# Kernel optimization log

Measured on AMD Instinct MI355X. Metric: run time of the kernel, lower is better.

Reference implementation:

```python
import jax, jax.numpy as jnp
import numpy as np

D_MODEL = 1024
N_HEADS = 16
HEAD_DIM = D_MODEL // N_HEADS


def setup_inputs() -> dict:
    key = jax.random.key(0)
    k0, k1, k2, k3, k4, k5 = jax.random.split(key, 6)
    s = 1.0 / np.sqrt(D_MODEL)
    return {
        "q": jax.random.normal(k0, (2, 2048, D_MODEL), dtype=jnp.float32),
        "Wq": jax.random.normal(k1, (D_MODEL, D_MODEL), dtype=jnp.float32) * s,
        "Wk": jax.random.normal(k2, (D_MODEL, D_MODEL), dtype=jnp.float32) * s,
        "Wv": jax.random.normal(k3, (D_MODEL, D_MODEL), dtype=jnp.float32) * s,
        "Wo": jax.random.normal(k4, (D_MODEL, D_MODEL), dtype=jnp.float32) * s,
        "bo": jax.random.normal(k5, (D_MODEL,), dtype=jnp.float32) * 0.01,
    }


def _split_heads(x):
    b, s, _ = x.shape
    return x.reshape(b, s, N_HEADS, HEAD_DIM).transpose(0, 2, 1, 3)  # [b,h,s,d]


def reference(q, Wq, Wk, Wv, Wo, bo):
    # self-attention: k = v = q
    qh = _split_heads(q @ Wq)  # [b,h,s,d]
    kh = _split_heads(q @ Wk)
    vh = _split_heads(q @ Wv)
    scale = 1.0 / np.sqrt(HEAD_DIM).astype(np.float32)
    scores = jnp.einsum("bhqd,bhkd->bhqk", qh, kh) * scale
    attn = jax.nn.softmax(scores, axis=-1)
    ctx = jnp.einsum("bhqk,bhkd->bhqd", attn, vh)
    b, h, s, d = ctx.shape
    ctx = ctx.transpose(0, 2, 1, 3).reshape(b, s, h * d)
    return ctx @ Wo + bo
```

## Files before the change

kernel.cpp:

```cpp
#include <hip/hip_runtime.h>
#include <cstdint>

typedef unsigned short u16;
typedef __bf16 bf16x8 __attribute__((ext_vector_type(8)));
typedef __bf16 bf16x2 __attribute__((ext_vector_type(2)));
typedef float floatx4 __attribute__((ext_vector_type(4)));
typedef unsigned short u16x4 __attribute__((ext_vector_type(4)));
typedef unsigned short u16x8 __attribute__((ext_vector_type(8)));

#define MFMA16(a, b, c) __builtin_amdgcn_mfma_f32_16x16x32_bf16((a), (b), (c), 0, 0, 0)
#define QSCALE_LOG2E 0.18033688011112042f


typedef __attribute__((address_space(3))) void as3_void;
typedef __attribute__((address_space(1))) void as1_void;

static __device__ __forceinline__ void async_load16(const void* g, void* l) {
  __builtin_amdgcn_global_load_lds((as1_void*)(uintptr_t)g, (as3_void*)(uintptr_t)l,
                                   16, 0, 0);
}

static __device__ __forceinline__ u16 f2bf(float f) {
  union { float f; unsigned int u; } v; v.f = f;
  unsigned int u = v.u;
  u += 0x7fffu + ((u >> 16) & 1u);
  return (u16)(u >> 16);
}

static __device__ __forceinline__ u16x4 pack_bf4(float a, float b, float c, float d) {
#if __has_builtin(__builtin_amdgcn_cvt_pk_bf16_f32)
  union { u16x4 v4; bf16x2 v2[2]; } u;
  u.v2[0] = __builtin_amdgcn_cvt_pk_bf16_f32(a, b);
  u.v2[1] = __builtin_amdgcn_cvt_pk_bf16_f32(c, d);
  return u.v4;
#else
  u16x4 r; r[0] = f2bf(a); r[1] = f2bf(b); r[2] = f2bf(c); r[3] = f2bf(d);
  return r;
#endif
}

static __device__ __forceinline__ float fast_exp2(float x) {
#if __has_builtin(__builtin_amdgcn_exp2f)
  return __builtin_amdgcn_exp2f(x);
#else
  return exp2f(x);
#endif
}


__global__ __launch_bounds__(256) void prep_kernel(
    const float* __restrict__ w0, const float* __restrict__ w1,
    const float* __restrict__ w2, const float* __restrict__ w3,
    u16* __restrict__ wout,
    const float* __restrict__ xin, u16* __restrict__ xout) {
  if (blockIdx.z == 4) {
    int blk = blockIdx.y * 16 + blockIdx.x;
    size_t base = (size_t)blk * 16384 + (size_t)threadIdx.x * 8;
#pragma unroll
    for (int r = 0; r < 8; r++) {
      size_t i = base + (size_t)r * 2048;
      float4 a = *(const float4*)(xin + i);
      float4 b = *(const float4*)(xin + i + 4);
      u16x8 o;
      o[0] = f2bf(a.x); o[1] = f2bf(a.y); o[2] = f2bf(a.z); o[3] = f2bf(a.w);
      o[4] = f2bf(b.x); o[5] = f2bf(b.y); o[6] = f2bf(b.z); o[7] = f2bf(b.w);
      *(u16x8*)(xout + i) = o;
    }
    return;
  }
  __shared__ u16 t[64][65];
  const float* in = (blockIdx.z == 0) ? w0 : (blockIdx.z == 1) ? w1
                    : (blockIdx.z == 2) ? w2 : w3;
  u16* oz = wout + (size_t)blockIdx.z * (1024 * 1024);
  const int tid = threadIdx.x;
  const int x = tid & 63, y0 = tid >> 6;
  const int bx = blockIdx.x * 64, by = blockIdx.y * 64;
#pragma unroll
  for (int p = 0; p < 16; p++) {
    int y = y0 + p * 4;
    t[y][x] = f2bf(in[(size_t)(by + y) * 1024 + bx + x]);
  }
  __syncthreads();
#pragma unroll
  for (int p = 0; p < 16; p++) {
    int r = y0 + p * 4;
    oz[(size_t)(bx + r) * 1024 + by + x] = t[x][r];
  }
}


__global__ __launch_bounds__(256, 3) void gemm_bt_kernel(
    const u16* __restrict__ A, const u16* __restrict__ BT,
    const float* __restrict__ bias, void* __restrict__ out,
    u16* __restrict__ outVT,
    int M, int N, int K, int mode) {
  __shared__ u16 As[128 * 32];
  __shared__ u16 Bs[128 * 32];
  const int tid = threadIdx.x;
  const int w = tid >> 6, lane = tid & 63;
  const int bm = blockIdx.y * 128, bn = blockIdx.x * 128;
  const int z = blockIdx.z;
  const u16* Bz = BT + (size_t)z * N * K;

  const int c0 = w * 2, c1 = c0 + 1;
  const int mA0 = c0 * 16 + (lane >> 2), mA1 = c1 * 16 + (lane >> 2);
  const int kg0 = (lane & 3) ^ ((mA0 >> 1) & 3);
  const int kg1 = (lane & 3) ^ ((mA1 >> 1) & 3);
  const u16* agp0 = A + (size_t)(bm + mA0) * K + kg0 * 8;
  const u16* agp1 = A + (size_t)(bm + mA1) * K + kg1 * 8;
  const u16* bgp0 = Bz + (size_t)(bn + mA0) * K + kg0 * 8;
  const u16* bgp1 = Bz + (size_t)(bn + mA1) * K + kg1 * 8;
  u16* ald0 = As + c0 * 512; u16* ald1 = As + c1 * 512;
  u16* bld0 = Bs + c0 * 512; u16* bld1 = Bs + c1 * 512;

  const int wm = (w >> 1) * 64, wn = (w & 1) * 64;
  floatx4 acc[4][4] = {};

  int a_off[4], b_off[4];
#pragma unroll
  for (int i = 0; i < 4; i++) {
    int m = wm + i * 16 + (lane & 15);
    a_off[i] = m * 32 + (((lane >> 4) ^ ((m >> 1) & 3)) * 8);
    int n = wn + i * 16 + (lane & 15);
    b_off[i] = n * 32 + (((lane >> 4) ^ ((n >> 1) & 3)) * 8);
  }

  for (int k0 = 0; k0 < K; k0 += 32) {
    __syncthreads();
    async_load16(agp0 + k0, ald0);
    async_load16(agp1 + k0, ald1);
    async_load16(bgp0 + k0, bld0);
    async_load16(bgp1 + k0, bld1);
    __syncthreads();
    bf16x8 af[4], bf[4];
#pragma unroll
    for (int i = 0; i < 4; i++) af[i] = *(const bf16x8*)(As + a_off[i]);
#pragma unroll
    for (int j = 0; j < 4; j++) bf[j] = *(const bf16x8*)(Bs + b_off[j]);
#pragma unroll
    for (int i = 0; i < 4; i++)
#pragma unroll
      for (int j = 0; j < 4; j++)
        acc[i][j] = MFMA16(af[i], bf[j], acc[i][j]);
  }

  const int roff = (lane >> 4) * 4;
  const int coff = lane & 15;
  if (mode == 0) {
    if (z == 2) {
#pragma unroll
      for (int i = 0; i < 4; i++) {
        int r0 = bm + wm + i * 16 + roff;
        int b = r0 >> 11, s = r0 & 2047;
#pragma unroll
        for (int j = 0; j < 4; j++) {
          int c = bn + wn + j * 16 + coff;
          int h = c >> 6, d = c & 63;
          u16x4 pk = pack_bf4(acc[i][j][0], acc[i][j][1], acc[i][j][2], acc[i][j][3]);
          *(u16x4*)(outVT + ((size_t)(b * 16 + h) * 64 + d) * 2048 + s) = pk;
        }
      }
    } else {
      const float sc = (z == 0) ? QSCALE_LOG2E : 1.0f;
      u16* outz = (u16*)out + (size_t)z * M * N;
#pragma unroll
      for (int i = 0; i < 4; i++) {
        int r0 = bm + wm + i * 16 + roff;
#pragma unroll
        for (int j = 0; j < 4; j++) {
          int c = bn + wn + j * 16 + coff;
#pragma unroll
          for (int r = 0; r < 4; r++)
            outz[(size_t)(r0 + r) * N + c] = f2bf(acc[i][j][r] * sc);
        }
      }
    }
  } else {
    float* outf = (float*)out;
#pragma unroll
    for (int i = 0; i < 4; i++) {
      int r0 = bm + wm + i * 16 + roff;
#pragma unroll
      for (int j = 0; j < 4; j++) {
        int c = bn + wn + j * 16 + coff;
        float bv = bias[c];
#pragma unroll
        for (int r = 0; r < 4; r++)
          outf[(size_t)(r0 + r) * N + c] = acc[i][j][r] + bv;
      }
    }
  }
}


__global__ __launch_bounds__(256, 2) void attn_kernel(
    const u16* __restrict__ Q, const u16* __restrict__ Kx,
    const u16* __restrict__ VT, u16* __restrict__ ctx) {
  __shared__ u16 Ks[128 * 64];
  __shared__ u16 Vs[64 * 128];
  __shared__ u16 Ps[4][32 * 136];
  const int tid = threadIdx.x;
  const int w = tid >> 6, lane = tid & 63;
  const int bid = blockIdx.x;
  const int bh = (bid >> 7) * 8 + (bid & 7);
  const int q0 = ((bid >> 3) & 15) * 128;
  const int b = bh >> 4, h = bh & 15;
  const u16* Qh = Q + (size_t)b * 2048 * 1024 + h * 64;
  const u16* Kh = Kx + (size_t)b * 2048 * 1024 + h * 64;
  const u16* Vh = VT + (size_t)bh * 64 * 2048;

  const int qbase = q0 + w * 32;
  bf16x8 qf[2][2];
#pragma unroll
  for (int qt = 0; qt < 2; qt++)
#pragma unroll
    for (int ks = 0; ks < 2; ks++)
      qf[qt][ks] = *(const bf16x8*)(Qh + (size_t)(qbase + qt * 16 + (lane & 15)) * 1024 +
                                    ks * 32 + (lane >> 4) * 8);

  bf16x8 onesf;
#pragma unroll
  for (int i = 0; i < 8; i++) onesf[i] = (__bf16)1.0f;
  const floatx4 zero4 = {};

  const u16* kgp[4]; const u16* vgp[4];
  u16* kld[4]; u16* vld[4];
#pragma unroll
  for (int i = 0; i < 4; i++) {
    int c = w * 4 + i;
    int sl = c * 8 + (lane >> 3);
    int dg = (lane & 7) ^ (lane >> 3);
    kgp[i] = Kh + (size_t)sl * 1024 + dg * 8;
    kld[i] = Ks + c * 512;
    int dl = c * 4 + (lane >> 4);
    int sg = (lane & 15) ^ (dl & 15);
    vgp[i] = Vh + (size_t)dl * 2048 + sg * 8;
    vld[i] = Vs + c * 512;
  }

  const int slot_k0 = (lane >> 4) ^ (lane & 7);
  const int slot_k1 = (4 + (lane >> 4)) ^ (lane & 7);
  const u16* kf0_base = Ks + (lane & 15) * 64 + slot_k0 * 8;
  const u16* kf1_base = Ks + (lane & 15) * 64 + slot_k1 * 8;

  floatx4 o[2][4] = {};
  floatx4 lacc[2] = {};
  u16* Pw = Ps[w];

  for (int t = 0; t < 16; t++) {
    const int k0 = t * 128;
    __syncthreads();
#pragma unroll
    for (int i = 0; i < 4; i++) {
      async_load16(kgp[i] + (size_t)k0 * 1024, kld[i]);
      async_load16(vgp[i] + k0, vld[i]);
    }
    __syncthreads();

#pragma unroll
    for (int si = 0; si < 8; si++) {
      bf16x8 kf0 = *(const bf16x8*)(kf0_base + si * 1024);
      bf16x8 kf1 = *(const bf16x8*)(kf1_base + si * 1024);
      floatx4 st0 = MFMA16(kf0, qf[0][0], zero4);
      st0 = MFMA16(kf1, qf[0][1], st0);
      floatx4 st1 = MFMA16(kf0, qf[1][0], zero4);
      st1 = MFMA16(kf1, qf[1][1], st1);
      u16x4 pk0 = pack_bf4(fast_exp2(st0[0]), fast_exp2(st0[1]),
                           fast_exp2(st0[2]), fast_exp2(st0[3]));
      u16x4 pk1 = pack_bf4(fast_exp2(st1[0]), fast_exp2(st1[1]),
                           fast_exp2(st1[2]), fast_exp2(st1[3]));
      *(u16x4*)(Pw + (lane & 15) * 136 + si * 16 + (lane >> 4) * 4) = pk0;
      *(u16x4*)(Pw + (16 + (lane & 15)) * 136 + si * 16 + (lane >> 4) * 4) = pk1;
    }

#pragma unroll
    for (int ks = 0; ks < 4; ks++) {
      bf16x8 vf[4];
#pragma unroll
      for (int jt = 0; jt < 4; jt++) {
        int d = jt * 16 + (lane & 15);
        int slot = ((ks * 4) + (lane >> 4)) ^ (d & 15);
        vf[jt] = *(const bf16x8*)(Vs + d * 128 + slot * 8);
      }
#pragma unroll
      for (int qt = 0; qt < 2; qt++) {
        bf16x8 pf = *(const bf16x8*)(Pw + (qt * 16 + (lane & 15)) * 136 +
                                     ks * 32 + (lane >> 4) * 8);
#pragma unroll
        for (int jt = 0; jt < 4; jt++)
          o[qt][jt] = MFMA16(pf, vf[jt], o[qt][jt]);
        lacc[qt] = MFMA16(pf, onesf, lacc[qt]);
      }
    }
  }

#pragma unroll
  for (int qt = 0; qt < 2; qt++)
#pragma unroll
    for (int r = 0; r < 4; r++) {
      float inv = 1.0f / lacc[qt][r];
      int s = qbase + qt * 16 + (lane >> 4) * 4 + r;
#pragma unroll
      for (int j = 0; j < 4; j++) {
        int c = h * 64 + j * 16 + (lane & 15);
        ctx[(size_t)(b * 2048 + s) * 1024 + c] = f2bf(o[qt][j][r] * inv);
      }
    }
}


extern "C" void kernel_launch(void* const* d_in, const int* in_sizes, int n_in,
                              void* d_out, int out_size, void* d_ws, size_t ws_size,
                              hipStream_t stream) {
  (void)in_sizes; (void)n_in; (void)out_size; (void)ws_size;
  const float* x  = (const float*)d_in[0];
  const float* Wq = (const float*)d_in[1];
  const float* Wk = (const float*)d_in[2];
  const float* Wv = (const float*)d_in[3];
  const float* Wo = (const float*)d_in[4];
  const float* bo = (const float*)d_in[5];
  u16* ws = (u16*)d_ws;
  const size_t MM = 1024 * 1024;
  u16* WT  = ws;
  u16* WoT = ws + 3 * MM;
  u16* Xb  = ws + 4 * MM;
  u16* QKV = ws + 8 * MM;
  u16* VTp = ws + 20 * MM;
  u16* CTX = ws + 24 * MM;

  dim3 blk(256);
  prep_kernel<<<dim3(16, 16, 5), blk, 0, stream>>>(Wq, Wk, Wv, Wo, WT, x, Xb);
  gemm_bt_kernel<<<dim3(8, 32, 3), blk, 0, stream>>>(Xb, WT, nullptr, QKV, VTp,
                                                     4096, 1024, 1024, 0);
  attn_kernel<<<dim3(512, 1, 1), blk, 0, stream>>>(QKV, QKV + 4 * MM, VTp, CTX);
  gemm_bt_kernel<<<dim3(8, 32, 1), blk, 0, stream>>>(CTX, WoT, bo, d_out, nullptr,
                                                     4096, 1024, 1024, 1);
}
```

Before: 194.5 us.

## Split attention key tile into halves to shrink P buffer and raise occupancy

The 128-key tile loop is split into two 64-key halves. Each half computes scores, exponentiates, writes P to LDS, then does the PV MFMAs. This halves the per-wave P scratch buffer (row stride 136 to 72) and lowers shared memory per block, and the launch bound is raised from 2 to 3 blocks per CU for more latency hiding. In exchange, the PV stage of one half depends directly on that half's P writes, and the tighter register budget may cause spills.

```diff
diff --git a/kernel.cpp b/kernel.cpp
--- a/kernel.cpp
+++ b/kernel.cpp
@@ -193,12 +193,12 @@
 }
 
 
-__global__ __launch_bounds__(256, 2) void attn_kernel(
+__global__ __launch_bounds__(256, 3) void attn_kernel(
     const u16* __restrict__ Q, const u16* __restrict__ Kx,
     const u16* __restrict__ VT, u16* __restrict__ ctx) {
   __shared__ u16 Ks[128 * 64];
   __shared__ u16 Vs[64 * 128];
-  __shared__ u16 Ps[4][32 * 136];
+  __shared__ u16 Ps[4][32 * 72];
   const int tid = threadIdx.x;
   const int w = tid >> 6, lane = tid & 63;
   const int bid = blockIdx.x;
@@ -246,6 +246,9 @@
   floatx4 o[2][4] = {};
   floatx4 lacc[2] = {};
   u16* Pw = Ps[w];
+  const int qrow0 = (lane & 15) * 72;
+  const int qrow1 = (16 + (lane & 15)) * 72;
+  const int quad = lane >> 4;
 
   for (int t = 0; t < 16; t++) {
     const int k0 = t * 128;
@@ -258,38 +261,44 @@
     __syncthreads();
 
 #pragma unroll
-    for (int si = 0; si < 8; si++) {
-      bf16x8 kf0 = *(const bf16x8*)(kf0_base + si * 1024);
-      bf16x8 kf1 = *(const bf16x8*)(kf1_base + si * 1024);
-      floatx4 st0 = MFMA16(kf0, qf[0][0], zero4);
-      st0 = MFMA16(kf1, qf[0][1], st0);
-      floatx4 st1 = MFMA16(kf0, qf[1][0], zero4);
-      st1 = MFMA16(kf1, qf[1][1], st1);
-      u16x4 pk0 = pack_bf4(fast_exp2(st0[0]), fast_exp2(st0[1]),
-                           fast_exp2(st0[2]), fast_exp2(st0[3]));
-      u16x4 pk1 = pack_bf4(fast_exp2(st1[0]), fast_exp2(st1[1]),
-                           fast_exp2(st1[2]), fast_exp2(st1[3]));
-      *(u16x4*)(Pw + (lane & 15) * 136 + si * 16 + (lane >> 4) * 4) = pk0;
-      *(u16x4*)(Pw + (16 + (lane & 15)) * 136 + si * 16 + (lane >> 4) * 4) = pk1;
-    }
-
-#pragma unroll
-    for (int ks = 0; ks < 4; ks++) {
-      bf16x8 vf[4];
-#pragma unroll
-      for (int jt = 0; jt < 4; jt++) {
-        int d = jt * 16 + (lane & 15);
-        int slot = ((ks * 4) + (lane >> 4)) ^ (d & 15);
-        vf[jt] = *(const bf16x8*)(Vs + d * 128 + slot * 8);
-      }
-#pragma unroll
-      for (int qt = 0; qt < 2; qt++) {
-        bf16x8 pf = *(const bf16x8*)(Pw + (qt * 16 + (lane & 15)) * 136 +
-                                     ks * 32 + (lane >> 4) * 8);
-#pragma unroll
-        for (int jt = 0; jt < 4; jt++)
-          o[qt][jt] = MFMA16(pf, vf[jt], o[qt][jt]);
-        lacc[qt] = MFMA16(pf, onesf, lacc[qt]);
+    for (int hh = 0; hh < 2; hh++) {
+      floatx4 st0[4], st1[4];
+#pragma unroll
+      for (int si4 = 0; si4 < 4; si4++) {
+        int si = hh * 4 + si4;
+        bf16x8 kf0 = *(const bf16x8*)(kf0_base + si * 1024);
+        bf16x8 kf1 = *(const bf16x8*)(kf1_base + si * 1024);
+        st0[si4] = MFMA16(kf1, qf[0][1], MFMA16(kf0, qf[0][0], zero4));
+        st1[si4] = MFMA16(kf1, qf[1][1], MFMA16(kf0, qf[1][0], zero4));
+      }
+#pragma unroll
+      for (int si4 = 0; si4 < 4; si4++) {
+        u16x4 pk0 = pack_bf4(fast_exp2(st0[si4][0]), fast_exp2(st0[si4][1]),
+                             fast_exp2(st0[si4][2]), fast_exp2(st0[si4][3]));
+        u16x4 pk1 = pack_bf4(fast_exp2(st1[si4][0]), fast_exp2(st1[si4][1]),
+                             fast_exp2(st1[si4][2]), fast_exp2(st1[si4][3]));
+        *(u16x4*)(Pw + qrow0 + si4 * 16 + quad * 4) = pk0;
+        *(u16x4*)(Pw + qrow1 + si4 * 16 + quad * 4) = pk1;
+      }
+#pragma unroll
+      for (int ksl = 0; ksl < 2; ksl++) {
+        int kb = hh * 2 + ksl;
+        bf16x8 vf[4];
+#pragma unroll
+        for (int jt = 0; jt < 4; jt++) {
+          int d = jt * 16 + (lane & 15);
+          int slot = (kb * 4 + quad) ^ (d & 15);
+          vf[jt] = *(const bf16x8*)(Vs + d * 128 + slot * 8);
+        }
+#pragma unroll
+        for (int qt = 0; qt < 2; qt++) {
+          bf16x8 pf = *(const bf16x8*)(Pw + (qt * 16 + (lane & 15)) * 72 +
+                                       ksl * 32 + quad * 8);
+#pragma unroll
+          for (int jt = 0; jt < 4; jt++)
+            o[qt][jt] = MFMA16(pf, vf[jt], o[qt][jt]);
+          lacc[qt] = MFMA16(pf, onesf, lacc[qt]);
+        }
       }
     }
   }
@@ -299,7 +308,7 @@
 #pragma unroll
     for (int r = 0; r < 4; r++) {
       float inv = 1.0f / lacc[qt][r];
-      int s = qbase + qt * 16 + (lane >> 4) * 4 + r;
+      int s = qbase + qt * 16 + quad * 4 + r;
 #pragma unroll
       for (int j = 0; j < 4; j++) {
         int c = h * 64 + j * 16 + (lane & 15);
```

New measurement: 190.7 us. 2.0% less time.
